# Performance work log

Measured on AMD Instinct MI355X. Metric: run time of the kernel, lower is better.

The kernel has to match this reference:

```python
import jax, jax.numpy as jnp
import numpy as np

E = 8        # num_experts
K = 2        # num_experts_per_tok
H = 1024     # hidden_dim
F = 2816     # intermediate_dim
R = 256      # shared-core rank
B, S = 2, 1024


def setup_inputs() -> dict:
    key = jax.random.key(0)
    ks = jax.random.split(key, 12)
    inp = {
        "hidden_states": jax.random.normal(ks[0], (B, S, H), jnp.float32),
        "gate_w": jax.random.normal(ks[1], (H, E), jnp.float32) / np.sqrt(H),
        # gate_proj: hidden -> intermediate, factored W_e = Ug[e] @ Cg @ Vg[e]
        "Ug": jax.random.normal(ks[2], (E, H, R), jnp.float32) / np.sqrt(H),
        "Cg": jax.random.normal(ks[3], (R, R), jnp.float32) / np.sqrt(R),
        "Vg": jax.random.normal(ks[4], (E, R, F), jnp.float32) / np.sqrt(R),
        # up_proj: hidden -> intermediate
        "Uu": jax.random.normal(ks[5], (E, H, R), jnp.float32) / np.sqrt(H),
        "Cu": jax.random.normal(ks[6], (R, R), jnp.float32) / np.sqrt(R),
        "Vu": jax.random.normal(ks[7], (E, R, F), jnp.float32) / np.sqrt(R),
        # down_proj: intermediate -> hidden
        "Ud": jax.random.normal(ks[8], (E, F, R), jnp.float32) / np.sqrt(F),
        "Cd": jax.random.normal(ks[9], (R, R), jnp.float32) / np.sqrt(R),
        "Vd": jax.random.normal(ks[10], (E, R, H), jnp.float32) / np.sqrt(R),
    }
    return inp


def _moe_forward(x, gate_w, Ug, Cg, Vg, Uu, Cu, Vu, Ud, Cd, Vd):
    b, s, h = x.shape
    xf = x.reshape(-1, h)                       # [T, H]
    T = xf.shape[0]
    logits = xf @ gate_w                        # [T, E]
    probs = jax.nn.softmax(logits, axis=-1)
    w, idx = jax.lax.top_k(probs, K)            # [T, K]
    w = w / jnp.sum(w, axis=-1, keepdims=True)
    # dense combine weights: combine[t, e] = sum of renormalized routing
    # weights over top-k slots routed to expert e (scatter-add in torch code)
    combine = jnp.zeros((T, E), xf.dtype).at[jnp.arange(T)[:, None], idx].add(w)
    out = jnp.zeros_like(xf)
    for e in range(E):  # fixed small expert count
        g = (xf @ Ug[e]) @ Cg @ Vg[e]           # [T, F]
        u = (xf @ Uu[e]) @ Cu @ Vu[e]           # [T, F]
        a = jax.nn.silu(g) * u
        y = (a @ Ud[e]) @ Cd @ Vd[e]            # [T, H]
        out = out + combine[:, e:e + 1] * y
    return out.reshape(b, s, h)


def reference(hidden_states, gate_w, Ug, Cg, Vg, Uu, Cu, Vu, Ud, Cd, Vd):
    return _moe_forward(hidden_states, gate_w, Ug, Cg, Vg, Uu, Cu, Vu, Ud, Cd, Vd)
```

## Files before the change

### kernel.cpp

```cpp
#include <hip/hip_runtime.h>
#include <math.h>

constexpr int cE = 8;
constexpr int cH = 1024;
constexpr int cF = 2816;
constexpr int cR = 256;
constexpr int cT = 2048;
constexpr int ROWS = cT * 2;
constexpr int LDA = 40;

using short8  = __attribute__((ext_vector_type(8))) short;
using float4v = __attribute__((ext_vector_type(4))) float;
#define MFMA16 __builtin_amdgcn_mfma_f32_16x16x32_bf16

__device__ __forceinline__ unsigned short f2bf(float f) {
  union { float f; unsigned u; } v; v.f = f;
  unsigned r = v.u + 0x7fffu + ((v.u >> 16) & 1u);
  return (unsigned short)(r >> 16);
}
__device__ __forceinline__ float bf2f(unsigned short s) {
  union { unsigned u; float f; } v; v.u = (unsigned)s << 16; return v.f;
}

__device__ __forceinline__ void store_bf8(unsigned short* dst, float4 a, float4 b) {
  union { unsigned short u[8]; uint4 v; } t;
  t.u[0] = f2bf(a.x); t.u[1] = f2bf(a.y); t.u[2] = f2bf(a.z); t.u[3] = f2bf(a.w);
  t.u[4] = f2bf(b.x); t.u[5] = f2bf(b.y); t.u[6] = f2bf(b.z); t.u[7] = f2bf(b.w);
  *reinterpret_cast<uint4*>(dst) = t.v;
}

__device__ __forceinline__ void gld16(const unsigned short* g, unsigned short* l) {
  __builtin_amdgcn_global_load_lds(
      (const __attribute__((address_space(1))) void*)g,
      (__attribute__((address_space(3))) void*)l, 16, 0, 0);
}

__global__ __launch_bounds__(256) void k_gating(
    const float* __restrict__ x, const float* __restrict__ gw,
    unsigned short* __restrict__ xb, int* __restrict__ et,
    float* __restrict__ wt)
{
  const int tid = threadIdx.x;
  const int wid = tid >> 6, lane = tid & 63;
  const int t = blockIdx.x * 4 + wid;
  const float* xr = x + (long)t * cH + lane * 16;
  float4 v0 = *reinterpret_cast<const float4*>(xr);
  float4 v1 = *reinterpret_cast<const float4*>(xr + 4);
  float4 v2 = *reinterpret_cast<const float4*>(xr + 8);
  float4 v3 = *reinterpret_cast<const float4*>(xr + 12);
  store_bf8(xb + (long)t * cH + lane * 16, v0, v1);
  store_bf8(xb + (long)t * cH + lane * 16 + 8, v2, v3);
  float xv[16];
  *reinterpret_cast<float4*>(&xv[0])  = v0;
  *reinterpret_cast<float4*>(&xv[4])  = v1;
  *reinterpret_cast<float4*>(&xv[8])  = v2;
  *reinterpret_cast<float4*>(&xv[12]) = v3;
  const float* g = gw + (long)lane * 16 * cE;
  float l[cE];
#pragma unroll
  for (int e = 0; e < cE; ++e) l[e] = 0.f;
#pragma unroll
  for (int i = 0; i < 16; ++i) {
    float4 ga = *reinterpret_cast<const float4*>(g + i * cE);
    float4 gb = *reinterpret_cast<const float4*>(g + i * cE + 4);
    float xi = xv[i];
    l[0] += xi * ga.x; l[1] += xi * ga.y; l[2] += xi * ga.z; l[3] += xi * ga.w;
    l[4] += xi * gb.x; l[5] += xi * gb.y; l[6] += xi * gb.z; l[7] += xi * gb.w;
  }
#pragma unroll
  for (int m = 1; m < 64; m <<= 1)
#pragma unroll
    for (int e = 0; e < cE; ++e)
      l[e] += __shfl_xor(l[e], m, 64);
  if (lane == 0) {
    int i0 = 0; float m0 = l[0];
#pragma unroll
    for (int e = 1; e < cE; ++e) if (l[e] > m0) { m0 = l[e]; i0 = e; }
    int i1 = -1; float m1 = -1e30f;
#pragma unroll
    for (int e = 0; e < cE; ++e) if (e != i0 && l[e] > m1) { m1 = l[e]; i1 = e; }
    float w0 = 1.f / (1.f + expf(m1 - m0));
    et[t * 2 + 0] = i0;  et[t * 2 + 1] = i1;
    wt[t * 2 + 0] = w0;  wt[t * 2 + 1] = 1.f - w0;
  }
}

__global__ __launch_bounds__(256) void k_lists(
    const int* __restrict__ et, int* __restrict__ rowmap,
    int* __restrict__ cnt, int* __restrict__ off)
{
  __shared__ int c[cE], p[cE], o[cE];
  const int tid = threadIdx.x;
  if (tid < cE) { c[tid] = 0; p[tid] = 0; }
  __syncthreads();
  for (int i = tid; i < ROWS; i += 256) atomicAdd(&c[et[i]], 1);
  __syncthreads();
  if (tid == 0) {
    int s = 0;
    for (int e = 0; e < cE; ++e) { o[e] = s; s += c[e]; }
  }
  __syncthreads();
  for (int i = tid; i < ROWS; i += 256) {
    int e = et[i];
    int slot = atomicAdd(&p[e], 1);
    rowmap[i] = o[e] + slot;
  }
  if (tid < cE) { cnt[tid] = c[tid]; off[tid] = o[tid]; }
}

__global__ __launch_bounds__(256) void k_tconv(
    const float* __restrict__ in, unsigned short* __restrict__ out, int P, int Q)
{
  __shared__ float tile[32][33];
  const long es = (long)P * Q;
  const int e = blockIdx.z;
  in += e * es; out += e * es;
  const int c0 = blockIdx.x * 32, r0 = blockIdx.y * 32;
  const int tid = threadIdx.x;
  const int r = tid >> 3, c4 = (tid & 7) * 4;
  float4 v = *reinterpret_cast<const float4*>(in + (long)(r0 + r) * Q + c0 + c4);
  tile[r][c4 + 0] = v.x; tile[r][c4 + 1] = v.y;
  tile[r][c4 + 2] = v.z; tile[r][c4 + 3] = v.w;
  __syncthreads();
  const int cc = tid >> 3, rr4 = (tid & 7) * 4;
  ushort4 o;
  o.x = f2bf(tile[rr4 + 0][cc]);
  o.y = f2bf(tile[rr4 + 1][cc]);
  o.z = f2bf(tile[rr4 + 2][cc]);
  o.w = f2bf(tile[rr4 + 3][cc]);
  *reinterpret_cast<ushort4*>(out + (long)(c0 + cc) * P + r0 + rr4) = o;
}

__global__ __launch_bounds__(256, 2) void k_foldm(
    const unsigned short* __restrict__ A, long sA,
    const float* __restrict__ B, long sB,
    unsigned short* __restrict__ D, long sD, int ldd)
{
  __shared__ __align__(16) unsigned short As[128 * LDA], Bs[64 * LDA];
  const int e = blockIdx.z;
  A += e * sA; B += e * sB; D += e * sD;
  const int m0 = blockIdx.y * 128, n0 = blockIdx.x * 64;
  const int tid = threadIdx.x;
  const int sr = tid >> 2, sk = (tid & 3) * 8;
  const unsigned short* a0 = A + (long)(m0 + sr) * 256 + sk;
  const unsigned short* a1 = a0 + (long)64 * 256;
  const float* br = B + (long)(n0 + sr) * 256 + sk;
  uint4 rA0, rA1; float4 rB0, rB1;
  auto load_slice = [&](int k0) {
    rA0 = *reinterpret_cast<const uint4*>(a0 + k0);
    rA1 = *reinterpret_cast<const uint4*>(a1 + k0);
    rB0 = *reinterpret_cast<const float4*>(br + k0);
    rB1 = *reinterpret_cast<const float4*>(br + k0 + 4);
  };
  load_slice(0);
  const int wid = tid >> 6, lane = tid & 63;
  const int wm = (wid >> 1) * 64, wn = (wid & 1) * 32;
  const int fr = lane & 15, fq = lane >> 4;
  float4v zf = {0.f, 0.f, 0.f, 0.f};
  float4v acc[4][2];
#pragma unroll
  for (int i = 0; i < 4; ++i) { acc[i][0] = zf; acc[i][1] = zf; }
  for (int k0 = 0; k0 < 256; k0 += 32) {
    *reinterpret_cast<uint4*>(&As[sr * LDA + sk]) = rA0;
    *reinterpret_cast<uint4*>(&As[(sr + 64) * LDA + sk]) = rA1;
    store_bf8(&Bs[sr * LDA + sk], rB0, rB1);
    if (k0 + 32 < 256) load_slice(k0 + 32);
    __syncthreads();
    short8 af[4], bf[2];
#pragma unroll
    for (int mi = 0; mi < 4; ++mi)
      af[mi] = *reinterpret_cast<const short8*>(&As[(wm + mi * 16 + fr) * LDA + fq * 8]);
#pragma unroll
    for (int nj = 0; nj < 2; ++nj)
      bf[nj] = *reinterpret_cast<const short8*>(&Bs[(wn + nj * 16 + fr) * LDA + fq * 8]);
#pragma unroll
    for (int mi = 0; mi < 4; ++mi)
#pragma unroll
      for (int nj = 0; nj < 2; ++nj)
        acc[mi][nj] = MFMA16(af[mi], bf[nj], acc[mi][nj], 0, 0, 0);
    __syncthreads();
  }
#pragma unroll
  for (int mi = 0; mi < 4; ++mi)
#pragma unroll
    for (int r = 0; r < 4; ++r) {
      int m = m0 + wm + mi * 16 + fq * 4 + r;
#pragma unroll
      for (int nj = 0; nj < 2; ++nj)
        D[(long)m * ldd + n0 + wn + nj * 16 + fr] = f2bf(acc[mi][nj][r]);
    }
}

__global__ __launch_bounds__(256, 2) void k_t1d(
    const unsigned short* __restrict__ xb, const unsigned short* __restrict__ b1t,
    unsigned short* __restrict__ t1, const int* __restrict__ et,
    const int* __restrict__ rowmap)
{
  __shared__ __align__(16) unsigned short As[128 * 64];
  __shared__ __align__(16) unsigned short Bs[128 * 64];
  const int tid = threadIdx.x;
  const int wid = tid >> 6, lane = tid & 63;
  const int m0 = blockIdx.y * 128;
  const int nb = blockIdx.x;
  const int srow = wid * 32 + (lane >> 3);
  const int scol = (lane & 7) * 8;
  const unsigned short* gA = xb + (long)(m0 + srow) * cH + scol;
  const unsigned short* gB = b1t + (long)(nb * 128 + srow) * cH + scol;
  unsigned short* lA = As + wid * 32 * 64;
  unsigned short* lB = Bs + wid * 32 * 64;
  const int wm = (wid >> 1) * 64, wn = (wid & 1) * 64;
  const int fr = lane & 15, fq = lane >> 4;
  float4v zf = {0.f, 0.f, 0.f, 0.f};
  float4v acc[4][4];
#pragma unroll
  for (int i = 0; i < 4; ++i)
#pragma unroll
    for (int j = 0; j < 4; ++j) acc[i][j] = zf;
  for (int k0 = 0; k0 < cH; k0 += 64) {
#pragma unroll
    for (int j = 0; j < 4; ++j) {
      gld16(gA + k0 + (long)j * 8 * cH, lA + j * 8 * 64);
      gld16(gB + k0 + (long)j * 8 * cH, lB + j * 8 * 64);
    }
    __syncthreads();
#pragma unroll
    for (int ks = 0; ks < 2; ++ks) {
      short8 af[4], bf[4];
#pragma unroll
      for (int mi = 0; mi < 4; ++mi)
        af[mi] = *reinterpret_cast<const short8*>(
            &As[(wm + mi * 16 + fr) * 64 + ks * 32 + fq * 8]);
#pragma unroll
      for (int nj = 0; nj < 4; ++nj)
        bf[nj] = *reinterpret_cast<const short8*>(
            &Bs[(wn + nj * 16 + fr) * 64 + ks * 32 + fq * 8]);
#pragma unroll
      for (int mi = 0; mi < 4; ++mi)
#pragma unroll
        for (int nj = 0; nj < 4; ++nj)
          acc[mi][nj] = MFMA16(af[mi], bf[nj], acc[mi][nj], 0, 0, 0);
    }
    __syncthreads();
  }
  const int e_t = nb >> 2;
  const int colbase = (nb & 3) * 128 + wn;
#pragma unroll
  for (int mi = 0; mi < 4; ++mi)
#pragma unroll
    for (int r = 0; r < 4; ++r) {
      int t = m0 + wm + mi * 16 + fq * 4 + r;
      int crow = -1;
      if (et[2 * t] == e_t) crow = rowmap[2 * t];
      else if (et[2 * t + 1] == e_t) crow = rowmap[2 * t + 1];
      if (crow >= 0) {
#pragma unroll
        for (int nj = 0; nj < 4; ++nj)
          t1[(long)crow * 512 + colbase + nj * 16 + fr] = f2bf(acc[mi][nj][r]);
      }
    }
}

__global__ __launch_bounds__(256, 2) void k_act(
    const unsigned short* __restrict__ t1,
    const unsigned short* __restrict__ vgT, const unsigned short* __restrict__ vuT,
    unsigned short* __restrict__ a, const int* __restrict__ cnt,
    const int* __restrict__ off)
{
  __shared__ __align__(16) unsigned short Ag[128 * 32], Au[128 * 32];
  __shared__ __align__(16) unsigned short Bg[64 * 32],  Bu[64 * 32];
  const int e = blockIdx.z, c = cnt[e], o = off[e];
  const int m0 = blockIdx.y * 128;
  if (m0 >= c) return;
  const int n0 = blockIdx.x * 64;
  const int tid = threadIdx.x;
  const int wid = tid >> 6, lane = tid & 63;
  const int sr16 = lane >> 2, sc = (lane & 3) * 8;
  const int ra0 = o + min(m0 + wid * 32 + sr16, c - 1);
  const int ra1 = o + min(m0 + wid * 32 + 16 + sr16, c - 1);
  const unsigned short* gAg0 = t1 + (long)ra0 * 512 + sc;
  const unsigned short* gAg1 = t1 + (long)ra1 * 512 + sc;
  const unsigned short* gBg = vgT + (long)e * cF * 256 + (long)(n0 + wid * 16 + sr16) * 256 + sc;
  const unsigned short* gBu = vuT + (long)e * cF * 256 + (long)(n0 + wid * 16 + sr16) * 256 + sc;
  unsigned short* lAg = Ag + wid * 32 * 32;
  unsigned short* lAu = Au + wid * 32 * 32;
  unsigned short* lBg = Bg + wid * 16 * 32;
  unsigned short* lBu = Bu + wid * 16 * 32;
  const int wm = (wid >> 1) * 64, wn = (wid & 1) * 32;
  const int fr = lane & 15, fq = lane >> 4;
  float4v zf = {0.f, 0.f, 0.f, 0.f};
  float4v accg[4][2], accu[4][2];
#pragma unroll
  for (int i = 0; i < 4; ++i) { accg[i][0] = zf; accg[i][1] = zf; accu[i][0] = zf; accu[i][1] = zf; }
  for (int k0 = 0; k0 < 256; k0 += 32) {
    gld16(gAg0 + k0, lAg);
    gld16(gAg1 + k0, lAg + 16 * 32);
    gld16(gAg0 + 256 + k0, lAu);
    gld16(gAg1 + 256 + k0, lAu + 16 * 32);
    gld16(gBg + k0, lBg);
    gld16(gBu + k0, lBu);
    __syncthreads();
    short8 ag[4], au[4], bg[2], bu[2];
#pragma unroll
    for (int mi = 0; mi < 4; ++mi) {
      ag[mi] = *reinterpret_cast<const short8*>(&Ag[(wm + mi * 16 + fr) * 32 + fq * 8]);
      au[mi] = *reinterpret_cast<const short8*>(&Au[(wm + mi * 16 + fr) * 32 + fq * 8]);
    }
#pragma unroll
    for (int nj = 0; nj < 2; ++nj) {
      bg[nj] = *reinterpret_cast<const short8*>(&Bg[(wn + nj * 16 + fr) * 32 + fq * 8]);
      bu[nj] = *reinterpret_cast<const short8*>(&Bu[(wn + nj * 16 + fr) * 32 + fq * 8]);
    }
#pragma unroll
    for (int mi = 0; mi < 4; ++mi)
#pragma unroll
      for (int nj = 0; nj < 2; ++nj) {
        accg[mi][nj] = MFMA16(ag[mi], bg[nj], accg[mi][nj], 0, 0, 0);
        accu[mi][nj] = MFMA16(au[mi], bu[nj], accu[mi][nj], 0, 0, 0);
      }
    __syncthreads();
  }
#pragma unroll
  for (int mi = 0; mi < 4; ++mi)
#pragma unroll
    for (int r = 0; r < 4; ++r) {
      int row = m0 + wm + mi * 16 + fq * 4 + r;
      if (row < c) {
#pragma unroll
        for (int nj = 0; nj < 2; ++nj) {
          float g = accg[mi][nj][r];
          float u = accu[mi][nj][r];
          float s = g / (1.f + expf(-g)) * u;
          a[(long)(o + row) * cF + n0 + wn + nj * 16 + fr] = f2bf(s);
        }
      }
    }
}

__global__ __launch_bounds__(256) void k_t3(
    const unsigned short* __restrict__ a, const unsigned short* __restrict__ udT,
    float* __restrict__ t3p, const int* __restrict__ cnt,
    const int* __restrict__ off)
{
  __shared__ __align__(16) unsigned short As[64 * 64], Bs[64 * 64];
  const int e = blockIdx.z, c = cnt[e], o = off[e];
  const int m0 = blockIdx.y * 64;
  if (m0 >= c) return;
  const int n0 = (blockIdx.x & 3) * 64;
  const int ksp = blockIdx.x >> 2;
  const int kbase = ksp * 704;
  const int tid = threadIdx.x;
  const int wid = tid >> 6, lane = tid & 63;
  const int sr8 = lane >> 3, sc = (lane & 7) * 8;
  const int ra0 = o + min(m0 + wid * 16 + sr8, c - 1);
  const int ra1 = o + min(m0 + wid * 16 + 8 + sr8, c - 1);
  const unsigned short* gA0 = a + (long)ra0 * cF + kbase + sc;
  const unsigned short* gA1 = a + (long)ra1 * cF + kbase + sc;
  const unsigned short* gB  = udT + (long)e * 256 * cF + (long)(n0 + wid * 16 + sr8) * cF + kbase + sc;
  unsigned short* lA = As + wid * 16 * 64;
  unsigned short* lB = Bs + wid * 16 * 64;
  const int wm = (wid >> 1) * 32, wn = (wid & 1) * 32;
  const int fr = lane & 15, fq = lane >> 4;
  float4v zf = {0.f, 0.f, 0.f, 0.f};
  float4v acc[2][2] = {{zf, zf}, {zf, zf}};
  for (int k0 = 0; k0 < 704; k0 += 64) {
    gld16(gA0 + k0, lA);
    gld16(gA1 + k0, lA + 8 * 64);
    gld16(gB + k0, lB);
    gld16(gB + (long)8 * cF + k0, lB + 8 * 64);
    __syncthreads();
#pragma unroll
    for (int ks = 0; ks < 2; ++ks) {
      short8 af[2], bf[2];
#pragma unroll
      for (int mi = 0; mi < 2; ++mi)
        af[mi] = *reinterpret_cast<const short8*>(
            &As[(wm + mi * 16 + fr) * 64 + ks * 32 + fq * 8]);
#pragma unroll
      for (int nj = 0; nj < 2; ++nj)
        bf[nj] = *reinterpret_cast<const short8*>(
            &Bs[(wn + nj * 16 + fr) * 64 + ks * 32 + fq * 8]);
#pragma unroll
      for (int mi = 0; mi < 2; ++mi)
#pragma unroll
        for (int nj = 0; nj < 2; ++nj)
          acc[mi][nj] = MFMA16(af[mi], bf[nj], acc[mi][nj], 0, 0, 0);
    }
    __syncthreads();
  }
  float* dstbase = t3p + (long)ksp * ROWS * 256;
#pragma unroll
  for (int mi = 0; mi < 2; ++mi)
#pragma unroll
    for (int r = 0; r < 4; ++r) {
      int row = m0 + wm + mi * 16 + fq * 4 + r;
      if (row < c) {
        float* dst = dstbase + (long)(o + row) * 256 + n0 + wn;
#pragma unroll
        for (int nj = 0; nj < 2; ++nj)
          dst[nj * 16 + fr] = acc[mi][nj][r];
      }
    }
}

__global__ __launch_bounds__(256) void k_red(
    const float* __restrict__ t3p, unsigned short* __restrict__ t3b)
{
  const long psz = (long)ROWS * 256;
  long i = ((long)blockIdx.x * 256 + threadIdx.x) * 8;
  float4 s0 = *reinterpret_cast<const float4*>(t3p + i);
  float4 s1 = *reinterpret_cast<const float4*>(t3p + i + 4);
#pragma unroll
  for (int q = 1; q < 4; ++q) {
    float4 a0 = *reinterpret_cast<const float4*>(t3p + q * psz + i);
    float4 a1 = *reinterpret_cast<const float4*>(t3p + q * psz + i + 4);
    s0.x += a0.x; s0.y += a0.y; s0.z += a0.z; s0.w += a0.w;
    s1.x += a1.x; s1.y += a1.y; s1.z += a1.z; s1.w += a1.w;
  }
  store_bf8(t3b + i, s0, s1);
}

__global__ __launch_bounds__(256, 2) void k_y(
    const unsigned short* __restrict__ t3b, const unsigned short* __restrict__ vd2t,
    unsigned short* __restrict__ y, const int* __restrict__ cnt,
    const int* __restrict__ off)
{
  __shared__ __align__(16) unsigned short As[128 * 32], Bs[64 * 32];
  const int e = blockIdx.z, c = cnt[e], o = off[e];
  const int m0 = blockIdx.y * 128;
  if (m0 >= c) return;
  const int n0 = blockIdx.x * 64;
  const int tid = threadIdx.x;
  const int wid = tid >> 6, lane = tid & 63;
  const int sr16 = lane >> 2, sc = (lane & 3) * 8;
  const int ra0 = o + min(m0 + wid * 32 + sr16, c - 1);
  const int ra1 = o + min(m0 + wid * 32 + 16 + sr16, c - 1);
  const unsigned short* gA0 = t3b + (long)ra0 * 256 + sc;
  const unsigned short* gA1 = t3b + (long)ra1 * 256 + sc;
  const unsigned short* gB  = vd2t + (long)e * cH * 256 + (long)(n0 + wid * 16 + sr16) * 256 + sc;
  unsigned short* lA = As + wid * 32 * 32;
  unsigned short* lB = Bs + wid * 16 * 32;
  const int wm = (wid >> 1) * 64, wn = (wid & 1) * 32;
  const int fr = lane & 15, fq = lane >> 4;
  float4v zf = {0.f, 0.f, 0.f, 0.f};
  float4v acc[4][2];
#pragma unroll
  for (int i = 0; i < 4; ++i) { acc[i][0] = zf; acc[i][1] = zf; }
  for (int k0 = 0; k0 < 256; k0 += 32) {
    gld16(gA0 + k0, lA);
    gld16(gA1 + k0, lA + 16 * 32);
    gld16(gB + k0, lB);
    __syncthreads();
    short8 af[4], bf[2];
#pragma unroll
    for (int mi = 0; mi < 4; ++mi)
      af[mi] = *reinterpret_cast<const short8*>(&As[(wm + mi * 16 + fr) * 32 + fq * 8]);
#pragma unroll
    for (int nj = 0; nj < 2; ++nj)
      bf[nj] = *reinterpret_cast<const short8*>(&Bs[(wn + nj * 16 + fr) * 32 + fq * 8]);
#pragma unroll
    for (int mi = 0; mi < 4; ++mi)
#pragma unroll
      for (int nj = 0; nj < 2; ++nj)
        acc[mi][nj] = MFMA16(af[mi], bf[nj], acc[mi][nj], 0, 0, 0);
    __syncthreads();
  }
#pragma unroll
  for (int mi = 0; mi < 4; ++mi)
#pragma unroll
    for (int r = 0; r < 4; ++r) {
      int row = m0 + wm + mi * 16 + fq * 4 + r;
      if (row < c) {
#pragma unroll
        for (int nj = 0; nj < 2; ++nj)
          y[(long)(o + row) * cH + n0 + wn + nj * 16 + fr] = f2bf(acc[mi][nj][r]);
      }
    }
}

__global__ __launch_bounds__(256) void k_combine(
    const unsigned short* __restrict__ y, const float* __restrict__ wt,
    const int* __restrict__ rowmap, float* __restrict__ out)
{
  const int tid = threadIdx.x;
  const int t = blockIdx.x * 2 + (tid >> 7);
  const int h = (tid & 127) * 8;
  const int r0 = rowmap[2 * t], r1 = rowmap[2 * t + 1];
  const float w0 = wt[2 * t], w1 = wt[2 * t + 1];
  union { uint4 v; unsigned short s[8]; } ua, ub;
  ua.v = *reinterpret_cast<const uint4*>(y + (long)r0 * cH + h);
  ub.v = *reinterpret_cast<const uint4*>(y + (long)r1 * cH + h);
  float o[8];
#pragma unroll
  for (int i = 0; i < 8; ++i)
    o[i] = w0 * bf2f(ua.s[i]) + w1 * bf2f(ub.s[i]);
  float* dst = out + (long)t * cH + h;
  *reinterpret_cast<float4*>(dst)     = make_float4(o[0], o[1], o[2], o[3]);
  *reinterpret_cast<float4*>(dst + 4) = make_float4(o[4], o[5], o[6], o[7]);
}

extern "C" void kernel_launch(void* const* d_in, const int* in_sizes, int n_in,
                              void* d_out, int out_size, void* d_ws, size_t ws_size,
                              hipStream_t stream)
{
  const float* x  = (const float*)d_in[0];
  const float* gw = (const float*)d_in[1];
  const float* Ug = (const float*)d_in[2];
  const float* Cg = (const float*)d_in[3];
  const float* Vg = (const float*)d_in[4];
  const float* Uu = (const float*)d_in[5];
  const float* Cu = (const float*)d_in[6];
  const float* Vu = (const float*)d_in[7];
  const float* Ud = (const float*)d_in[8];
  const float* Cd = (const float*)d_in[9];
  const float* Vd = (const float*)d_in[10];
  float* out = (float*)d_out;

  char* w = (char*)d_ws;
  unsigned short* vgT = (unsigned short*)w;
  float*          t3p = (float*)w;
  unsigned short* t3b = (unsigned short*)(w + (long)4 * ROWS * 256 * 4);
  w += (long)cE * cF * 256 * 2;
  unsigned short* b1t = (unsigned short*)w;  w += (long)cE * 512 * 1024 * 2;
  unsigned short* vd2t = (unsigned short*)w; w += (long)cE * cH * 256 * 2;
  unsigned short* vuT = (unsigned short*)w;
  unsigned short* yb  = (unsigned short*)w;  w += (long)cE * cF * 256 * 2;
  unsigned short* udT = (unsigned short*)w;  w += (long)cE * 256 * cF * 2;
  unsigned short* VdT = (unsigned short*)w;
  unsigned short* xb  = (unsigned short*)w;  w += (long)cE * cH * 256 * 2;
  unsigned short* CgT = (unsigned short*)w;  w += (long)cR * cR * 2;
  unsigned short* CuT = (unsigned short*)w;  w += (long)cR * cR * 2;
  unsigned short* t1  = (unsigned short*)w;  w += (long)ROWS * 512 * 2;
  unsigned short* ab  = (unsigned short*)w;  w += (long)ROWS * cF * 2;
  float* wt   = (float*)w; w += ROWS * 4;
  int* et     = (int*)w; w += ROWS * 4;
  int* rowmap = (int*)w; w += ROWS * 4;
  int* cnt = (int*)w; w += cE * 4;
  int* off = (int*)w; w += cE * 4;

  k_tconv<<<dim3(cR / 32, cR / 32, 1), dim3(256), 0, stream>>>(Cg, CgT, cR, cR);
  k_tconv<<<dim3(cR / 32, cR / 32, 1), dim3(256), 0, stream>>>(Cu, CuT, cR, cR);
  k_tconv<<<dim3(cH / 32, cR / 32, cE), dim3(256), 0, stream>>>(Vd, VdT, cR, cH);
  k_tconv<<<dim3(cF / 32, cR / 32, cE), dim3(256), 0, stream>>>(Vg, vgT, cR, cF);
  k_tconv<<<dim3(cF / 32, cR / 32, cE), dim3(256), 0, stream>>>(Vu, vuT, cR, cF);
  k_tconv<<<dim3(cR / 32, cF / 32, cE), dim3(256), 0, stream>>>(Ud, udT, cF, cR);
  k_foldm<<<dim3(cH / 64, cR / 128, cE), dim3(256), 0, stream>>>(
      CgT, 0, Ug, (long)cH * cR, b1t, (long)512 * 1024, cH);
  k_foldm<<<dim3(cH / 64, cR / 128, cE), dim3(256), 0, stream>>>(
      CuT, 0, Uu, (long)cH * cR, b1t + (long)256 * 1024, (long)512 * 1024, cH);
  k_foldm<<<dim3(cR / 64, cH / 128, cE), dim3(256), 0, stream>>>(
      VdT, (long)cH * cR, Cd, 0, vd2t, (long)cH * 256, cR);
  k_gating<<<dim3(cT / 4), dim3(256), 0, stream>>>(x, gw, xb, et, wt);
  k_lists<<<dim3(1), dim3(256), 0, stream>>>(et, rowmap, cnt, off);
  k_t1d<<<dim3(32, cT / 128), dim3(256), 0, stream>>>(xb, b1t, t1, et, rowmap);
  k_act<<<dim3(cF / 64, cT / 128, cE), dim3(256), 0, stream>>>(t1, vgT, vuT, ab, cnt, off);
  k_t3<<<dim3(16, cT / 64, cE), dim3(256), 0, stream>>>(ab, udT, t3p, cnt, off);
  k_red<<<dim3(ROWS * 256 / (256 * 8)), dim3(256), 0, stream>>>(t3p, t3b);
  k_y<<<dim3(cH / 64, cT / 128, cE), dim3(256), 0, stream>>>(t3b, vd2t, yb, cnt, off);
  k_combine<<<dim3(cT / 2), dim3(256), 0, stream>>>(yb, wt, rowmap, out);
}
```

Baseline: 310.3 us.

## Gather routed tokens for first projection and merge prep kernel launches

Replaces the dense first-stage GEMM, which computed every token against all eight experts' folded U·C matrices and then discarded the unrouted rows, with a gathered per-expert GEMM. It uses a new token list built in k_lists, so only routed rows are computed. The six transpose-convert launches are merged into one flat-grid kernel, and the two gate/up fold GEMMs into one launch, to cut launch overhead. The gathered A loads use indirect row pointers, which can reduce coalescing, and the smaller N tile lowers per-block reuse.

```diff
diff --git a/kernel.cpp b/kernel.cpp
--- a/kernel.cpp
+++ b/kernel.cpp
@@ -87,7 +87,7 @@
 
 __global__ __launch_bounds__(256) void k_lists(
     const int* __restrict__ et, int* __restrict__ rowmap,
-    int* __restrict__ cnt, int* __restrict__ off)
+    int* __restrict__ tok, int* __restrict__ cnt, int* __restrict__ off)
 {
   __shared__ int c[cE], p[cE], o[cE];
   const int tid = threadIdx.x;
@@ -103,20 +103,20 @@
   for (int i = tid; i < ROWS; i += 256) {
     int e = et[i];
     int slot = atomicAdd(&p[e], 1);
-    rowmap[i] = o[e] + slot;
+    int cr = o[e] + slot;
+    rowmap[i] = cr;
+    tok[cr] = i >> 1;
   }
   if (tid < cE) { cnt[tid] = c[tid]; off[tid] = o[tid]; }
 }
 
-__global__ __launch_bounds__(256) void k_tconv(
-    const float* __restrict__ in, unsigned short* __restrict__ out, int P, int Q)
-{
-  __shared__ float tile[32][33];
+__device__ __forceinline__ void tconv_tile(
+    const float* __restrict__ in, unsigned short* __restrict__ out,
+    int P, int Q, int e, int bx, int by, int tid, float (*tile)[33])
+{
   const long es = (long)P * Q;
-  const int e = blockIdx.z;
   in += e * es; out += e * es;
-  const int c0 = blockIdx.x * 32, r0 = blockIdx.y * 32;
-  const int tid = threadIdx.x;
+  const int c0 = bx * 32, r0 = by * 32;
   const int r = tid >> 3, c4 = (tid & 7) * 4;
   float4 v = *reinterpret_cast<const float4*>(in + (long)(r0 + r) * Q + c0 + c4);
   tile[r][c4 + 0] = v.x; tile[r][c4 + 1] = v.y;
@@ -131,16 +131,35 @@
   *reinterpret_cast<ushort4*>(out + (long)(c0 + cc) * P + r0 + rr4) = o;
 }
 
-__global__ __launch_bounds__(256, 2) void k_foldm(
-    const unsigned short* __restrict__ A, long sA,
-    const float* __restrict__ B, long sB,
-    unsigned short* __restrict__ D, long sD, int ldd)
-{
-  __shared__ __align__(16) unsigned short As[128 * LDA], Bs[64 * LDA];
-  const int e = blockIdx.z;
-  A += e * sA; B += e * sB; D += e * sD;
-  const int m0 = blockIdx.y * 128, n0 = blockIdx.x * 64;
-  const int tid = threadIdx.x;
+constexpr int TCONV_BLOCKS = 19072;
+__global__ __launch_bounds__(256) void k_tconv_all(
+    const float* __restrict__ Cg, unsigned short* __restrict__ CgT,
+    const float* __restrict__ Cu, unsigned short* __restrict__ CuT,
+    const float* __restrict__ Vd, unsigned short* __restrict__ VdT,
+    const float* __restrict__ Vg, unsigned short* __restrict__ vgT,
+    const float* __restrict__ Vu, unsigned short* __restrict__ vuT,
+    const float* __restrict__ Ud, unsigned short* __restrict__ udT)
+{
+  __shared__ float tile[32][33];
+  int b = blockIdx.x;
+  const float* in; unsigned short* out; int P, Q;
+  if (b < 64)         { in = Cg; out = CgT; P = 256;  Q = 256;  }
+  else if (b < 128)   { b -= 64;    in = Cu; out = CuT; P = 256;  Q = 256;  }
+  else if (b < 2176)  { b -= 128;   in = Vd; out = VdT; P = 256;  Q = 1024; }
+  else if (b < 7808)  { b -= 2176;  in = Vg; out = vgT; P = 256;  Q = 2816; }
+  else if (b < 13440) { b -= 7808;  in = Vu; out = vuT; P = 256;  Q = 2816; }
+  else                { b -= 13440; in = Ud; out = udT; P = 2816; Q = 256;  }
+  const int tpe = (P / 32) * (Q / 32);
+  const int e = b / tpe, rem = b % tpe;
+  const int bx = rem % (Q / 32), by = rem / (Q / 32);
+  tconv_tile(in, out, P, Q, e, bx, by, threadIdx.x, tile);
+}
+
+__device__ __forceinline__ void foldm_body(
+    const unsigned short* __restrict__ A, const float* __restrict__ B,
+    unsigned short* __restrict__ D, int ldd, int m0, int n0, int tid,
+    unsigned short* As, unsigned short* Bs)
+{
   const int sr = tid >> 2, sk = (tid & 3) * 8;
   const unsigned short* a0 = A + (long)(m0 + sr) * 256 + sk;
   const unsigned short* a1 = a0 + (long)64 * 256;
@@ -191,71 +210,93 @@
     }
 }
 
-__global__ __launch_bounds__(256, 2) void k_t1d(
+__global__ __launch_bounds__(256, 2) void k_foldm(
+    const unsigned short* __restrict__ A, long sA,
+    const float* __restrict__ B, long sB,
+    unsigned short* __restrict__ D, long sD, int ldd)
+{
+  __shared__ __align__(16) unsigned short As[128 * LDA], Bs[64 * LDA];
+  const int e = blockIdx.z;
+  foldm_body(A + e * sA, B + e * sB, D + e * sD, ldd,
+             blockIdx.y * 128, blockIdx.x * 64, threadIdx.x, As, Bs);
+}
+
+__global__ __launch_bounds__(256, 2) void k_foldm2(
+    const unsigned short* __restrict__ A0, const unsigned short* __restrict__ A1,
+    const float* __restrict__ B0, const float* __restrict__ B1,
+    unsigned short* __restrict__ D)
+{
+  __shared__ __align__(16) unsigned short As[128 * LDA], Bs[64 * LDA];
+  const int z = blockIdx.z, sel = z >> 3, e = z & 7;
+  const unsigned short* A = sel ? A1 : A0;
+  const float* B = (sel ? B1 : B0) + (long)e * cH * cR;
+  unsigned short* Dp = D + (long)e * 512 * 1024 + (long)sel * 256 * 1024;
+  foldm_body(A, B, Dp, cH, blockIdx.y * 128, blockIdx.x * 64, threadIdx.x, As, Bs);
+}
+
+__global__ __launch_bounds__(256, 2) void k_t1c(
     const unsigned short* __restrict__ xb, const unsigned short* __restrict__ b1t,
-    unsigned short* __restrict__ t1, const int* __restrict__ et,
-    const int* __restrict__ rowmap)
-{
-  __shared__ __align__(16) unsigned short As[128 * 64];
-  __shared__ __align__(16) unsigned short Bs[128 * 64];
+    unsigned short* __restrict__ t1, const int* __restrict__ tok,
+    const int* __restrict__ cnt, const int* __restrict__ off)
+{
+  __shared__ __align__(16) unsigned short As[128 * 64], Bs[64 * 64];
+  const int e = blockIdx.z, c = cnt[e], o = off[e];
+  const int m0 = blockIdx.y * 128;
+  if (m0 >= c) return;
+  const int n0 = blockIdx.x * 64;
   const int tid = threadIdx.x;
   const int wid = tid >> 6, lane = tid & 63;
-  const int m0 = blockIdx.y * 128;
-  const int nb = blockIdx.x;
-  const int srow = wid * 32 + (lane >> 3);
-  const int scol = (lane & 7) * 8;
-  const unsigned short* gA = xb + (long)(m0 + srow) * cH + scol;
-  const unsigned short* gB = b1t + (long)(nb * 128 + srow) * cH + scol;
+  const int sr8 = lane >> 3, sc = (lane & 7) * 8;
+  const unsigned short* gA[4];
+#pragma unroll
+  for (int j = 0; j < 4; ++j) {
+    int row = min(m0 + wid * 32 + j * 8 + sr8, c - 1);
+    gA[j] = xb + (long)tok[o + row] * cH + sc;
+  }
+  const unsigned short* gB = b1t + (long)e * 512 * 1024 +
+      (long)(n0 + wid * 16 + sr8) * 1024 + sc;
   unsigned short* lA = As + wid * 32 * 64;
-  unsigned short* lB = Bs + wid * 32 * 64;
-  const int wm = (wid >> 1) * 64, wn = (wid & 1) * 64;
+  unsigned short* lB = Bs + wid * 16 * 64;
+  const int wm = (wid >> 1) * 64, wn = (wid & 1) * 32;
   const int fr = lane & 15, fq = lane >> 4;
   float4v zf = {0.f, 0.f, 0.f, 0.f};
-  float4v acc[4][4];
-#pragma unroll
-  for (int i = 0; i < 4; ++i)
-#pragma unroll
-    for (int j = 0; j < 4; ++j) acc[i][j] = zf;
+  float4v acc[4][2];
+#pragma unroll
+  for (int i = 0; i < 4; ++i) { acc[i][0] = zf; acc[i][1] = zf; }
   for (int k0 = 0; k0 < cH; k0 += 64) {
 #pragma unroll
-    for (int j = 0; j < 4; ++j) {
-      gld16(gA + k0 + (long)j * 8 * cH, lA + j * 8 * 64);
-      gld16(gB + k0 + (long)j * 8 * cH, lB + j * 8 * 64);
-    }
+    for (int j = 0; j < 4; ++j) gld16(gA[j] + k0, lA + j * 8 * 64);
+    gld16(gB + k0, lB);
+    gld16(gB + (long)8 * 1024 + k0, lB + 8 * 64);
     __syncthreads();
 #pragma unroll
     for (int ks = 0; ks < 2; ++ks) {
-      short8 af[4], bf[4];
+      short8 af[4], bf[2];
 #pragma unroll
       for (int mi = 0; mi < 4; ++mi)
         af[mi] = *reinterpret_cast<const short8*>(
             &As[(wm + mi * 16 + fr) * 64 + ks * 32 + fq * 8]);
 #pragma unroll
-      for (int nj = 0; nj < 4; ++nj)
+      for (int nj = 0; nj < 2; ++nj)
         bf[nj] = *reinterpret_cast<const short8*>(
             &Bs[(wn + nj * 16 + fr) * 64 + ks * 32 + fq * 8]);
 #pragma unroll
       for (int mi = 0; mi < 4; ++mi)
 #pragma unroll
-        for (int nj = 0; nj < 4; ++nj)
+        for (int nj = 0; nj < 2; ++nj)
           acc[mi][nj] = MFMA16(af[mi], bf[nj], acc[mi][nj], 0, 0, 0);
     }
     __syncthreads();
   }
-  const int e_t = nb >> 2;
-  const int colbase = (nb & 3) * 128 + wn;
 #pragma unroll
   for (int mi = 0; mi < 4; ++mi)
 #pragma unroll
     for (int r = 0; r < 4; ++r) {
-      int t = m0 + wm + mi * 16 + fq * 4 + r;
-      int crow = -1;
-      if (et[2 * t] == e_t) crow = rowmap[2 * t];
-      else if (et[2 * t + 1] == e_t) crow = rowmap[2 * t + 1];
-      if (crow >= 0) {
-#pragma unroll
-        for (int nj = 0; nj < 4; ++nj)
-          t1[(long)crow * 512 + colbase + nj * 16 + fr] = f2bf(acc[mi][nj][r]);
+      int row = m0 + wm + mi * 16 + fq * 4 + r;
+      if (row < c) {
+#pragma unroll
+        for (int nj = 0; nj < 2; ++nj)
+          t1[(long)(o + row) * 512 + n0 + wn + nj * 16 + fr] = f2bf(acc[mi][nj][r]);
       }
     }
 }
@@ -534,24 +575,19 @@
   float* wt   = (float*)w; w += ROWS * 4;
   int* et     = (int*)w; w += ROWS * 4;
   int* rowmap = (int*)w; w += ROWS * 4;
+  int* tok    = (int*)w; w += ROWS * 4;
   int* cnt = (int*)w; w += cE * 4;
   int* off = (int*)w; w += cE * 4;
 
-  k_tconv<<<dim3(cR / 32, cR / 32, 1), dim3(256), 0, stream>>>(Cg, CgT, cR, cR);
-  k_tconv<<<dim3(cR / 32, cR / 32, 1), dim3(256), 0, stream>>>(Cu, CuT, cR, cR);
-  k_tconv<<<dim3(cH / 32, cR / 32, cE), dim3(256), 0, stream>>>(Vd, VdT, cR, cH);
-  k_tconv<<<dim3(cF / 32, cR / 32, cE), dim3(256), 0, stream>>>(Vg, vgT, cR, cF);
-  k_tconv<<<dim3(cF / 32, cR / 32, cE), dim3(256), 0, stream>>>(Vu, vuT, cR, cF);
-  k_tconv<<<dim3(cR / 32, cF / 32, cE), dim3(256), 0, stream>>>(Ud, udT, cF, cR);
-  k_foldm<<<dim3(cH / 64, cR / 128, cE), dim3(256), 0, stream>>>(
-      CgT, 0, Ug, (long)cH * cR, b1t, (long)512 * 1024, cH);
-  k_foldm<<<dim3(cH / 64, cR / 128, cE), dim3(256), 0, stream>>>(
-      CuT, 0, Uu, (long)cH * cR, b1t + (long)256 * 1024, (long)512 * 1024, cH);
+  k_tconv_all<<<dim3(TCONV_BLOCKS), dim3(256), 0, stream>>>(
+      Cg, CgT, Cu, CuT, Vd, VdT, Vg, vgT, Vu, vuT, Ud, udT);
+  k_foldm2<<<dim3(cH / 64, cR / 128, 16), dim3(256), 0, stream>>>(
+      CgT, CuT, Ug, Uu, b1t);
   k_foldm<<<dim3(cR / 64, cH / 128, cE), dim3(256), 0, stream>>>(
       VdT, (long)cH * cR, Cd, 0, vd2t, (long)cH * 256, cR);
   k_gating<<<dim3(cT / 4), dim3(256), 0, stream>>>(x, gw, xb, et, wt);
-  k_lists<<<dim3(1), dim3(256), 0, stream>>>(et, rowmap, cnt, off);
-  k_t1d<<<dim3(32, cT / 128), dim3(256), 0, stream>>>(xb, b1t, t1, et, rowmap);
+  k_lists<<<dim3(1), dim3(256), 0, stream>>>(et, rowmap, tok, cnt, off);
+  k_t1c<<<dim3(8, cT / 128, cE), dim3(256), 0, stream>>>(xb, b1t, t1, tok, cnt, off);
   k_act<<<dim3(cF / 64, cT / 128, cE), dim3(256), 0, stream>>>(t1, vgT, vuT, ab, cnt, off);
   k_t3<<<dim3(16, cT / 64, cE), dim3(256), 0, stream>>>(ab, udT, t3p, cnt, off);
   k_red<<<dim3(ROWS * 256 / (256 * 8)), dim3(256), 0, stream>>>(t3p, t3b);
```

Measured after the change: 293.0 us. 5.6% less time.
